# Kernel optimization log

Hardware: AMD Instinct MI355X
Metric: run time of the kernel (lower is better)

Reference implementation:

```python
import jax, jax.numpy as jnp
import numpy as np

B, S, D, H = 4, 2048, 1024, 16
DH = D // H
NEG = -1e9


def setup_inputs() -> dict:
    key = jax.random.key(0)
    ks = jax.random.split(key, 6)
    return {
        "q_raw": jax.random.normal(ks[0], (B, S, D), jnp.float32),
        "kv_raw": jax.random.normal(ks[1], (B, S, D), jnp.float32),
        "padding_mask": jnp.ones((B, S), jnp.int32),
        "Wq": jax.random.normal(ks[2], (D, D), jnp.float32) * 0.02,
        "Wk": jax.random.normal(ks[3], (D, D), jnp.float32) * 0.02,
        "Wv": jax.random.normal(ks[4], (D, D), jnp.float32) * 0.02,
        "Wo": jax.random.normal(ks[5], (D, D), jnp.float32) * 0.02,
    }


def _split_heads(x):
    # (B, S, D) -> (B, H, S, DH)
    return x.reshape(B, S, H, DH).transpose(0, 2, 1, 3)


def reference(q_raw, kv_raw, padding_mask, Wq, Wk, Wv, Wo):
    # nn.Linear (no bias): y = x @ W.T
    q = _split_heads(q_raw @ Wq.T)
    k = _split_heads(kv_raw @ Wk.T)
    v = _split_heads(kv_raw @ Wv.T)

    scale = 1.0 / jnp.sqrt(jnp.float32(DH))
    scores = jnp.einsum("bhqd,bhkd->bhqk", q, k) * scale  # (B,H,S,S)

    # padding mask: 0 -> masked (broadcast over query dim), as in torch code
    pad = (padding_mask == 0)[:, None, None, :]  # (B,1,1,S)
    scores = jnp.where(pad, NEG, scores)
    # causal mask (only applied when padding_mask given, matching original)
    causal = jnp.triu(jnp.ones((S, S), bool), k=1)  # (S,S)
    scores = jnp.where(causal[None, None], NEG, scores)

    w = jax.nn.softmax(scores, axis=-1)
    att = jnp.einsum("bhqk,bhkd->bhqd", w, v)  # (B,H,S,DH)
    att = att.transpose(0, 2, 1, 3).reshape(B, S, D)
    return att @ Wo.T
```

## Files before the change

kernel.cpp:

```cpp
#include <hip/hip_runtime.h>
#include <stdint.h>

typedef __attribute__((ext_vector_type(8))) short  short8;
typedef __attribute__((ext_vector_type(4))) float  f32x4;
typedef __attribute__((ext_vector_type(4))) unsigned short us4;

static __device__ __forceinline__ unsigned short f2bf(float x) {
  unsigned u = __builtin_bit_cast(unsigned, x);
  u += 0x7FFFu + ((u >> 16) & 1u);
  return (unsigned short)(u >> 16);
}

static __device__ __forceinline__ unsigned cvt_pk_bf16(float lo, float hi) {
  unsigned r;
  asm("v_cvt_pk_bf16_f32 %0, %1, %2" : "=v"(r) : "v"(lo), "v"(hi));
  return r;
}

template <int CTRL>
static __device__ __forceinline__ float maxdpp(float v) {
  int o = __builtin_amdgcn_update_dpp(0, __builtin_bit_cast(int, v), CTRL, 0xf, 0xf, false);
  return fmaxf(v, __builtin_bit_cast(float, o));
}
static __device__ __forceinline__ float rowmax16(float v) {
  v = maxdpp<0xB1>(v);
  v = maxdpp<0x4E>(v);
  v = maxdpp<0x141>(v);
  v = maxdpp<0x140>(v);
  return v;
}

__global__ __launch_bounds__(256) void cvt6(const float* __restrict__ q_raw,
                                            const float* __restrict__ kv_raw,
                                            const float* __restrict__ Wq,
                                            const float* __restrict__ Wk,
                                            const float* __restrict__ Wv,
                                            const float* __restrict__ Wo,
                                            unsigned short* __restrict__ qbf,
                                            unsigned short* __restrict__ kvbf,
                                            unsigned short* __restrict__ wbf) {
  const int y = blockIdx.y;
  const float* in;
  unsigned short* out;
  int n4;
  if (y == 0)      { in = q_raw;  out = qbf;  n4 = 2097152; }
  else if (y == 1) { in = kv_raw; out = kvbf; n4 = 2097152; }
  else {
    in  = (y == 2) ? Wq : (y == 3) ? Wk : (y == 4) ? Wv : Wo;
    out = wbf + (size_t)(y - 2) * 1048576;
    n4 = 262144;
  }
  int i = blockIdx.x * 256 + threadIdx.x;
  const int stride = gridDim.x * 256;
  for (; i < n4; i += stride) {
    f32x4 v = *((const f32x4*)in + i);
    us4 o = { f2bf(v[0]), f2bf(v[1]), f2bf(v[2]), f2bf(v[3]) };
    *((us4*)out + i) = o;
  }
}

__global__ __launch_bounds__(1024) void bias_kernel(const int* __restrict__ pm,
                                                    float* __restrict__ bias,
                                                    unsigned* __restrict__ flagmask) {
  __shared__ unsigned m;
  const int b = blockIdx.x, tid = threadIdx.x;
  if (tid == 0) m = 0;
  __syncthreads();
  const int i0 = b * 2048 + tid;
  const int z0 = pm[i0], z1 = pm[i0 + 1024];
  bias[i0]        = z0 ? 0.f : -1.0e9f;
  bias[i0 + 1024] = z1 ? 0.f : -1.0e9f;
  const int wv = tid >> 6;
  unsigned long long b0 = __ballot(z0 == 0);
  unsigned long long b1 = __ballot(z1 == 0);
  if ((tid & 63) == 0) {
    unsigned bits = (b0 ? (1u << wv) : 0u) | (b1 ? (1u << (wv + 16)) : 0u);
    if (bits) atomicOr(&m, bits);
  }
  __syncthreads();
  if (tid == 0) flagmask[b] = m;
}

static __device__ __forceinline__ void g2l16(const void* g, void* l) {
  __builtin_amdgcn_global_load_lds(
      (const __attribute__((address_space(1))) void*)g,
      (__attribute__((address_space(3))) void*)l, 16, 0, 0);
}

__global__ __launch_bounds__(256) void gemm_proj(const unsigned short* __restrict__ qbf,
                                                 const unsigned short* __restrict__ kvbf,
                                                 const unsigned short* __restrict__ wbf,
                                                 unsigned short* __restrict__ Qp,
                                                 unsigned short* __restrict__ Kp,
                                                 unsigned short* __restrict__ Vtp,
                                                 float qscale) {
  __shared__ unsigned short Alds[128 * 32];
  __shared__ unsigned short Blds[128 * 32];
  const int tid  = threadIdx.x;
  const int lane = tid & 63;
  const int w    = tid >> 6;
  const int g    = lane >> 4;
  const int li   = lane & 15;
  const int x = blockIdx.x;
  const int region = x >> 3;
  const int n0 = (x & 7) * 128;
  const int m0 = blockIdx.y * 128;
  const int wm = (w >> 1) * 64;
  const int wn = (w & 1) * 64;

  const unsigned short* A = (region == 0) ? qbf : kvbf;
  const unsigned short* W = wbf + (size_t)region * 1048576;

  int aoff[4], boff[4];
#pragma unroll
  for (int mi = 0; mi < 4; ++mi) {
    int row = wm + mi * 16 + li;
    aoff[mi] = row * 32 + (g ^ ((row >> 1) & 3)) * 8;
  }
#pragma unroll
  for (int ni = 0; ni < 4; ++ni) {
    int col = wn + ni * 16 + li;
    boff[ni] = col * 32 + (g ^ ((col >> 1) & 3)) * 8;
  }

  const int s1 = tid, s2 = 256 + tid;
  const int r1 = s1 >> 2, gc1 = (s1 & 3) ^ ((r1 >> 1) & 3);
  const int r2 = s2 >> 2, gc2 = (s2 & 3) ^ ((r2 >> 1) & 3);
  const unsigned short* gA1 = A + (size_t)(m0 + r1) * 1024 + gc1 * 8;
  const unsigned short* gA2 = A + (size_t)(m0 + r2) * 1024 + gc2 * 8;
  const unsigned short* gB1 = W + (size_t)(n0 + r1) * 1024 + gc1 * 8;
  const unsigned short* gB2 = W + (size_t)(n0 + r2) * 1024 + gc2 * 8;
  unsigned short* lA1 = &Alds[w * 512];
  unsigned short* lA2 = &Alds[2048 + w * 512];
  unsigned short* lB1 = &Blds[w * 512];
  unsigned short* lB2 = &Blds[2048 + w * 512];

  f32x4 acc[4][4] = {};

#pragma unroll 1
  for (int kt = 0; kt < 32; ++kt) {
    g2l16(gA1, lA1); g2l16(gA2, lA2);
    g2l16(gB1, lB1); g2l16(gB2, lB2);
    gA1 += 32; gA2 += 32; gB1 += 32; gB2 += 32;
    asm volatile("s_waitcnt vmcnt(0)" ::: "memory");
    __syncthreads();
    short8 af[4], bf[4];
#pragma unroll
    for (int mi = 0; mi < 4; ++mi) af[mi] = *(const short8*)&Alds[aoff[mi]];
#pragma unroll
    for (int ni = 0; ni < 4; ++ni) bf[ni] = *(const short8*)&Blds[boff[ni]];
#pragma unroll
    for (int mi = 0; mi < 4; ++mi)
#pragma unroll
      for (int ni = 0; ni < 4; ++ni)
        acc[mi][ni] = __builtin_amdgcn_mfma_f32_16x16x32_bf16(af[mi], bf[ni], acc[mi][ni], 0, 0, 0);
    __syncthreads();
  }

  if (region == 2) {
#pragma unroll
    for (int mi = 0; mi < 4; ++mi) {
      int mb = m0 + wm + mi * 16 + g * 4;
      int bb = mb >> 11, s = mb & 2047;
#pragma unroll
      for (int ni = 0; ni < 4; ++ni) {
        int n = n0 + wn + ni * 16 + li;
        us4 pk = { f2bf(acc[mi][ni][0]), f2bf(acc[mi][ni][1]),
                   f2bf(acc[mi][ni][2]), f2bf(acc[mi][ni][3]) };
        *(us4*)&Vtp[(size_t)(bb * 1024 + n) * 2048 + s] = pk;
      }
    }
  } else {
    unsigned short* C = (region == 0) ? Qp : Kp;
    const float sc = (region == 0) ? qscale : 1.0f;
#pragma unroll
    for (int mi = 0; mi < 4; ++mi) {
      int mb = m0 + wm + mi * 16 + g * 4;
#pragma unroll
      for (int ni = 0; ni < 4; ++ni) {
        int n = n0 + wn + ni * 16 + li;
#pragma unroll
        for (int r = 0; r < 4; ++r)
          C[(size_t)(mb + r) * 1024 + n] = f2bf(acc[mi][ni][r] * sc);
      }
    }
  }
}

__global__ __launch_bounds__(256) void gemm_out(const unsigned short* __restrict__ A,
                                                const unsigned short* __restrict__ W,
                                                float* __restrict__ C) {
  __shared__ unsigned short Alds[128 * 32];
  __shared__ unsigned short Blds[128 * 32];
  const int tid  = threadIdx.x;
  const int lane = tid & 63;
  const int w    = tid >> 6;
  const int g    = lane >> 4;
  const int li   = lane & 15;
  const int m0 = blockIdx.y * 128;
  const int n0 = blockIdx.x * 128;
  const int wm = (w >> 1) * 64;
  const int wn = (w & 1) * 64;

  int aoff[4], boff[4];
#pragma unroll
  for (int mi = 0; mi < 4; ++mi) {
    int row = wm + mi * 16 + li;
    aoff[mi] = row * 32 + (g ^ ((row >> 1) & 3)) * 8;
  }
#pragma unroll
  for (int ni = 0; ni < 4; ++ni) {
    int col = wn + ni * 16 + li;
    boff[ni] = col * 32 + (g ^ ((col >> 1) & 3)) * 8;
  }

  const int s1 = tid, s2 = 256 + tid;
  const int r1 = s1 >> 2, gc1 = (s1 & 3) ^ ((r1 >> 1) & 3);
  const int r2 = s2 >> 2, gc2 = (s2 & 3) ^ ((r2 >> 1) & 3);
  const unsigned short* gA1 = A + (size_t)(m0 + r1) * 1024 + gc1 * 8;
  const unsigned short* gA2 = A + (size_t)(m0 + r2) * 1024 + gc2 * 8;
  const unsigned short* gB1 = W + (size_t)(n0 + r1) * 1024 + gc1 * 8;
  const unsigned short* gB2 = W + (size_t)(n0 + r2) * 1024 + gc2 * 8;
  unsigned short* lA1 = &Alds[w * 512];
  unsigned short* lA2 = &Alds[2048 + w * 512];
  unsigned short* lB1 = &Blds[w * 512];
  unsigned short* lB2 = &Blds[2048 + w * 512];

  f32x4 acc[4][4] = {};

#pragma unroll 1
  for (int kt = 0; kt < 32; ++kt) {
    g2l16(gA1, lA1); g2l16(gA2, lA2);
    g2l16(gB1, lB1); g2l16(gB2, lB2);
    gA1 += 32; gA2 += 32; gB1 += 32; gB2 += 32;
    asm volatile("s_waitcnt vmcnt(0)" ::: "memory");
    __syncthreads();
    short8 af[4], bf[4];
#pragma unroll
    for (int mi = 0; mi < 4; ++mi) af[mi] = *(const short8*)&Alds[aoff[mi]];
#pragma unroll
    for (int ni = 0; ni < 4; ++ni) bf[ni] = *(const short8*)&Blds[boff[ni]];
#pragma unroll
    for (int mi = 0; mi < 4; ++mi)
#pragma unroll
      for (int ni = 0; ni < 4; ++ni)
        acc[mi][ni] = __builtin_amdgcn_mfma_f32_16x16x32_bf16(af[mi], bf[ni], acc[mi][ni], 0, 0, 0);
    __syncthreads();
  }

#pragma unroll
  for (int mi = 0; mi < 4; ++mi) {
    int mb = m0 + wm + mi * 16 + g * 4;
#pragma unroll
    for (int ni = 0; ni < 4; ++ni) {
      int n = n0 + wn + ni * 16 + li;
#pragma unroll
      for (int r = 0; r < 4; ++r)
        C[(size_t)(mb + r) * 1024 + n] = acc[mi][ni][r];
    }
  }
}

__global__ __launch_bounds__(256, 4) void attn_kernel(const unsigned short* __restrict__ Qp,
                                                      const unsigned short* __restrict__ Kp,
                                                      const unsigned short* __restrict__ Vt,
                                                      const float* __restrict__ bias,
                                                      const unsigned* __restrict__ flagmask,
                                                      unsigned short* __restrict__ att) {
  __shared__ unsigned short Klds[2][64 * 64];
  __shared__ unsigned short Vlds[2][64 * 64];
  __shared__ unsigned short Plds[4][16 * 64];

  const int tid = threadIdx.x, lane = tid & 63, w = tid >> 6;
  const int g = lane >> 4, li = lane & 15;

  const int rid = blockIdx.x + (blockIdx.y << 4);
  const int xcd = rid & 7, kk = rid >> 3;
  const int bh = (kk & 7) | (xcd << 3);
  const int b = bh >> 4, h = bh & 15;
  const int tA = kk >> 3, tB = 31 - tA;
  const int nA = tA + 1, nB = tB + 1;

  const unsigned smask = flagmask[b];

  const int s1 = tid, s2 = tid + 256;
  const int r1 = s1 >> 3, c1 = (s1 & 7) ^ (r1 & 7);
  const int r2 = s2 >> 3, c2 = (s2 & 7) ^ (r2 & 7);
  const unsigned short* Kb1 = Kp + (size_t)(b * 2048 + r1) * 1024 + h * 64 + c1 * 8;
  const unsigned short* Kb2 = Kp + (size_t)(b * 2048 + r2) * 1024 + h * 64 + c2 * 8;
  const unsigned short* Vb1 = Vt + (size_t)(b * 1024 + h * 64 + r1) * 2048 + c1 * 8;
  const unsigned short* Vb2 = Vt + (size_t)(b * 1024 + h * 64 + r2) * 2048 + c2 * 8;

  int foff[2][4];
#pragma unroll
  for (int ks = 0; ks < 2; ++ks)
#pragma unroll
    for (int i = 0; i < 4; ++i)
      foff[ks][i] = (i * 16 + li) * 64 + (((ks * 4 + g) ^ (li & 7)) * 8);

  unsigned short* Pl = &Plds[w][0];
  const int swr = (li & 7) ^ (li >> 3);
  int poff[2];
#pragma unroll
  for (int ks = 0; ks < 2; ++ks) poff[ks] = li * 64 + ((ks * 4 + g) ^ swr) * 8;

  const float* bbase = bias + b * 2048 + li;

  short8 ones;
#pragma unroll
  for (int j = 0; j < 8; ++j) ones[j] = (short)0x3F80;

  int qw = tA * 64 + w * 16;
  short8 qfr[2];
#pragma unroll
  for (int ks = 0; ks < 2; ++ks)
    qfr[ks] = *(const short8*)&Qp[((size_t)(b * 2048 + qw + li)) * 1024 +
                                  h * 64 + ks * 32 + g * 8];

  f32x4 acco[4] = {};
  f32x4 lacc = {};
  float mrow[4] = {-3.0e38f, -3.0e38f, -3.0e38f, -3.0e38f};
  const f32x4 Z = {0.f, 0.f, 0.f, 0.f};

  auto stage = [&](int kt, int bufn) {
    const size_t ko = (size_t)kt * 65536, vo = (size_t)kt * 64;
    g2l16(Kb1 + ko, &Klds[bufn][w * 512]);
    g2l16(Kb2 + ko, &Klds[bufn][2048 + w * 512]);
    g2l16(Vb1 + vo, &Vlds[bufn][w * 512]);
    g2l16(Vb2 + vo, &Vlds[bufn][2048 + w * 512]);
  };

  auto body = [&](int kt, bool diag, int buf) {
    f32x4 s[4];
#pragma unroll
    for (int ni = 0; ni < 4; ++ni) {
      short8 kf = *(const short8*)&Klds[buf][foff[0][ni]];
      s[ni] = __builtin_amdgcn_mfma_f32_16x16x32_bf16(qfr[0], kf, Z, 0, 0, 0);
    }
#pragma unroll
    for (int ni = 0; ni < 4; ++ni) {
      short8 kf = *(const short8*)&Klds[buf][foff[1][ni]];
      s[ni] = __builtin_amdgcn_mfma_f32_16x16x32_bf16(qfr[1], kf, s[ni], 0, 0, 0);
    }
    if ((smask >> kt) & 1u) {
#pragma unroll
      for (int ni = 0; ni < 4; ++ni) {
        float bv = bbase[kt * 64 + ni * 16];
#pragma unroll
        for (int r = 0; r < 4; ++r) s[ni][r] += bv;
      }
    }
    if (diag) {
      const int q0 = qw + g * 4;
#pragma unroll
      for (int ni = 0; ni < 4; ++ni) {
        const int key = kt * 64 + ni * 16 + li;
#pragma unroll
        for (int r = 0; r < 4; ++r)
          if (key > q0 + r) s[ni][r] = -1.0e9f;
      }
    }
    float tm[4];
#pragma unroll
    for (int r = 0; r < 4; ++r)
      tm[r] = rowmax16(fmaxf(fmaxf(s[0][r], s[1][r]), fmaxf(s[2][r], s[3][r])));
    int need = 0;
#pragma unroll
    for (int r = 0; r < 4; ++r) need |= (tm[r] > mrow[r] + 8.0f) ? 1 : 0;
    if (__any(need)) {
#pragma unroll
      for (int r = 0; r < 4; ++r) {
        const float mn = fmaxf(mrow[r], tm[r]);
        const float al = __builtin_amdgcn_exp2f(mrow[r] - mn);
        mrow[r] = mn;
        lacc[r] *= al;
#pragma unroll
        for (int df = 0; df < 4; ++df) acco[df][r] *= al;
      }
    }
#pragma unroll
    for (int ni = 0; ni < 4; ++ni) {
#pragma unroll
      for (int h2 = 0; h2 < 2; ++h2) {
        float lo = __builtin_amdgcn_exp2f(s[ni][2 * h2]     - mrow[2 * h2]);
        float hi = __builtin_amdgcn_exp2f(s[ni][2 * h2 + 1] - mrow[2 * h2 + 1]);
        unsigned pk = cvt_pk_bf16(lo, hi);
        const int r0 = g * 4 + 2 * h2;
        const int ch = 2 * ni + (li >> 3);
        const int lo7 = li & 7;
        Pl[r0 * 64 + ((ch ^ ((r0 & 7) ^ (g >> 1))) * 8) + lo7] = (unsigned short)pk;
        const int rr = r0 + 1;
        Pl[rr * 64 + ((ch ^ ((rr & 7) ^ (g >> 1))) * 8) + lo7] = (unsigned short)(pk >> 16);
      }
    }
#pragma unroll
    for (int ks = 0; ks < 2; ++ks) {
      const short8 pa = *(const short8*)&Pl[poff[ks]];
      short8 vf[4];
#pragma unroll
      for (int df = 0; df < 4; ++df) vf[df] = *(const short8*)&Vlds[buf][foff[ks][df]];
#pragma unroll
      for (int df = 0; df < 4; ++df)
        acco[df] = __builtin_amdgcn_mfma_f32_16x16x32_bf16(pa, vf[df], acco[df], 0, 0, 0);
      lacc = __builtin_amdgcn_mfma_f32_16x16x32_bf16(pa, ones, lacc, 0, 0, 0);
    }
  };

  auto epilogue = [&]() {
    float inv[4];
#pragma unroll
    for (int r = 0; r < 4; ++r) inv[r] = __builtin_amdgcn_rcpf(lacc[r]);
    const int qb0 = qw + g * 4;
#pragma unroll
    for (int df = 0; df < 4; ++df) {
      const int d = h * 64 + df * 16 + li;
#pragma unroll
      for (int r = 0; r < 4; ++r)
        att[(size_t)(b * 2048 + qb0 + r) * 1024 + d] = f2bf(acco[df][r] * inv[r]);
    }
  };

  stage(0, 0);
  int buf = 0;

#pragma unroll 1
  for (int kt = 0; kt < nA; ++kt) {
    stage((kt + 1 < nA) ? kt + 1 : 0, buf ^ 1);
    asm volatile("s_waitcnt vmcnt(4)" ::: "memory");
    __builtin_amdgcn_s_barrier();
    body(kt, kt == nA - 1, buf);
    __builtin_amdgcn_s_barrier();
    buf ^= 1;
  }

  epilogue();
  qw = tB * 64 + w * 16;
#pragma unroll
  for (int ks = 0; ks < 2; ++ks)
    qfr[ks] = *(const short8*)&Qp[((size_t)(b * 2048 + qw + li)) * 1024 +
                                  h * 64 + ks * 32 + g * 8];
#pragma unroll
  for (int df = 0; df < 4; ++df) acco[df] = Z;
  lacc = Z;
#pragma unroll
  for (int r = 0; r < 4; ++r) mrow[r] = -3.0e38f;

#pragma unroll 1
  for (int kt = 0; kt < nB; ++kt) {
    if (kt + 1 < nB) {
      stage(kt + 1, buf ^ 1);
      asm volatile("s_waitcnt vmcnt(4)" ::: "memory");
    } else {
      asm volatile("s_waitcnt vmcnt(0)" ::: "memory");
    }
    __builtin_amdgcn_s_barrier();
    body(kt, kt == nB - 1, buf);
    __builtin_amdgcn_s_barrier();
    buf ^= 1;
  }

  epilogue();
}

extern "C" void kernel_launch(void* const* d_in, const int* in_sizes, int n_in,
                              void* d_out, int out_size, void* d_ws, size_t ws_size,
                              hipStream_t stream) {
  const float* q_raw  = (const float*)d_in[0];
  const float* kv_raw = (const float*)d_in[1];
  const int*   pmask  = (const int*)d_in[2];
  const float* Wq = (const float*)d_in[3];
  const float* Wk = (const float*)d_in[4];
  const float* Wv = (const float*)d_in[5];
  const float* Wo = (const float*)d_in[6];
  float* out = (float*)d_out;

  const size_t NEL = 8388608;
  const size_t WEL = 1048576;
  unsigned short* ws   = (unsigned short*)d_ws;
  unsigned short* qbf  = ws;
  unsigned short* kvbf = qbf + NEL;
  unsigned short* wbf  = kvbf + NEL;
  unsigned short* Qp   = wbf + 4 * WEL;
  unsigned short* Kp   = Qp + NEL;
  unsigned short* Vtp  = Kp + NEL;
  float*          bias = (float*)(Vtp + NEL);
  unsigned*       flagmask = (unsigned*)(bias + 8192);
  unsigned short* att  = qbf;

  const float sc = 0.125f * 1.44269504088896340736f;

  cvt6<<<dim3(512, 6), 256, 0, stream>>>(q_raw, kv_raw, Wq, Wk, Wv, Wo, qbf, kvbf, wbf);
  bias_kernel<<<4, 1024, 0, stream>>>(pmask, bias, flagmask);
  gemm_proj<<<dim3(24, 64), 256, 0, stream>>>(qbf, kvbf, wbf, Qp, Kp, Vtp, sc);
  attn_kernel<<<dim3(16, 64), 256, 0, stream>>>(Qp, Kp, Vtp, bias, flagmask, att);
  gemm_out<<<dim3(8, 64), 256, 0, stream>>>(att, wbf + 3 * WEL, out);
}
```

Baseline: 211.4 us.

## Double-buffer GEMM LDS loads and remap blocks for XCD-local L2 reuse

```diff
diff --git a/kernel.cpp b/kernel.cpp
--- a/kernel.cpp
+++ b/kernel.cpp
@@ -94,17 +94,20 @@
                                                  unsigned short* __restrict__ Kp,
                                                  unsigned short* __restrict__ Vtp,
                                                  float qscale) {
-  __shared__ unsigned short Alds[128 * 32];
-  __shared__ unsigned short Blds[128 * 32];
+  __shared__ unsigned short Alds[2][4096];
+  __shared__ unsigned short Blds[2][4096];
   const int tid  = threadIdx.x;
   const int lane = tid & 63;
   const int w    = tid >> 6;
   const int g    = lane >> 4;
   const int li   = lane & 15;
-  const int x = blockIdx.x;
-  const int region = x >> 3;
-  const int n0 = (x & 7) * 128;
-  const int m0 = blockIdx.y * 128;
+
+  const int l = blockIdx.x;
+  const int xcd = l & 7, j = l >> 3;
+  const int mstep = j & 7, rn = j >> 3;
+  const int region = rn >> 3;
+  const int n0 = (rn & 7) * 128;
+  const int m0 = (xcd * 8 + mstep) * 128;
   const int wm = (w >> 1) * 64;
   const int wn = (w & 1) * 64;
 
@@ -130,31 +133,37 @@
   const unsigned short* gA2 = A + (size_t)(m0 + r2) * 1024 + gc2 * 8;
   const unsigned short* gB1 = W + (size_t)(n0 + r1) * 1024 + gc1 * 8;
   const unsigned short* gB2 = W + (size_t)(n0 + r2) * 1024 + gc2 * 8;
-  unsigned short* lA1 = &Alds[w * 512];
-  unsigned short* lA2 = &Alds[2048 + w * 512];
-  unsigned short* lB1 = &Blds[w * 512];
-  unsigned short* lB2 = &Blds[2048 + w * 512];
 
   f32x4 acc[4][4] = {};
 
+  g2l16(gA1, &Alds[0][w * 512]); g2l16(gA2, &Alds[0][2048 + w * 512]);
+  g2l16(gB1, &Blds[0][w * 512]); g2l16(gB2, &Blds[0][2048 + w * 512]);
+  gA1 += 32; gA2 += 32; gB1 += 32; gB2 += 32;
+
+  int cur = 0;
 #pragma unroll 1
   for (int kt = 0; kt < 32; ++kt) {
-    g2l16(gA1, lA1); g2l16(gA2, lA2);
-    g2l16(gB1, lB1); g2l16(gB2, lB2);
-    gA1 += 32; gA2 += 32; gB1 += 32; gB2 += 32;
-    asm volatile("s_waitcnt vmcnt(0)" ::: "memory");
-    __syncthreads();
+    if (kt < 31) {
+      g2l16(gA1, &Alds[cur ^ 1][w * 512]); g2l16(gA2, &Alds[cur ^ 1][2048 + w * 512]);
+      g2l16(gB1, &Blds[cur ^ 1][w * 512]); g2l16(gB2, &Blds[cur ^ 1][2048 + w * 512]);
+      gA1 += 32; gA2 += 32; gB1 += 32; gB2 += 32;
+      asm volatile("s_waitcnt vmcnt(4)" ::: "memory");
+    } else {
+      asm volatile("s_waitcnt vmcnt(0)" ::: "memory");
+    }
+    __builtin_amdgcn_s_barrier();
     short8 af[4], bf[4];
 #pragma unroll
-    for (int mi = 0; mi < 4; ++mi) af[mi] = *(const short8*)&Alds[aoff[mi]];
-#pragma unroll
-    for (int ni = 0; ni < 4; ++ni) bf[ni] = *(const short8*)&Blds[boff[ni]];
+    for (int mi = 0; mi < 4; ++mi) af[mi] = *(const short8*)&Alds[cur][aoff[mi]];
+#pragma unroll
+    for (int ni = 0; ni < 4; ++ni) bf[ni] = *(const short8*)&Blds[cur][boff[ni]];
 #pragma unroll
     for (int mi = 0; mi < 4; ++mi)
 #pragma unroll
       for (int ni = 0; ni < 4; ++ni)
         acc[mi][ni] = __builtin_amdgcn_mfma_f32_16x16x32_bf16(af[mi], bf[ni], acc[mi][ni], 0, 0, 0);
-    __syncthreads();
+    __builtin_amdgcn_s_barrier();
+    cur ^= 1;
   }
 
   if (region == 2) {
@@ -190,15 +199,19 @@
 __global__ __launch_bounds__(256) void gemm_out(const unsigned short* __restrict__ A,
                                                 const unsigned short* __restrict__ W,
                                                 float* __restrict__ C) {
-  __shared__ unsigned short Alds[128 * 32];
-  __shared__ unsigned short Blds[128 * 32];
+  __shared__ unsigned short Alds[2][4096];
+  __shared__ unsigned short Blds[2][4096];
   const int tid  = threadIdx.x;
   const int lane = tid & 63;
   const int w    = tid >> 6;
   const int g    = lane >> 4;
   const int li   = lane & 15;
-  const int m0 = blockIdx.y * 128;
-  const int n0 = blockIdx.x * 128;
+
+  const int l = blockIdx.x;
+  const int xcd = l & 7, j = l >> 3;
+  const int mstep = j & 7, nt = j >> 3;
+  const int m0 = (xcd * 8 + mstep) * 128;
+  const int n0 = nt * 128;
   const int wm = (w >> 1) * 64;
   const int wn = (w & 1) * 64;
 
@@ -221,31 +234,37 @@
   const unsigned short* gA2 = A + (size_t)(m0 + r2) * 1024 + gc2 * 8;
   const unsigned short* gB1 = W + (size_t)(n0 + r1) * 1024 + gc1 * 8;
   const unsigned short* gB2 = W + (size_t)(n0 + r2) * 1024 + gc2 * 8;
-  unsigned short* lA1 = &Alds[w * 512];
-  unsigned short* lA2 = &Alds[2048 + w * 512];
-  unsigned short* lB1 = &Blds[w * 512];
-  unsigned short* lB2 = &Blds[2048 + w * 512];
 
   f32x4 acc[4][4] = {};
 
+  g2l16(gA1, &Alds[0][w * 512]); g2l16(gA2, &Alds[0][2048 + w * 512]);
+  g2l16(gB1, &Blds[0][w * 512]); g2l16(gB2, &Blds[0][2048 + w * 512]);
+  gA1 += 32; gA2 += 32; gB1 += 32; gB2 += 32;
+
+  int cur = 0;
 #pragma unroll 1
   for (int kt = 0; kt < 32; ++kt) {
-    g2l16(gA1, lA1); g2l16(gA2, lA2);
-    g2l16(gB1, lB1); g2l16(gB2, lB2);
-    gA1 += 32; gA2 += 32; gB1 += 32; gB2 += 32;
-    asm volatile("s_waitcnt vmcnt(0)" ::: "memory");
-    __syncthreads();
+    if (kt < 31) {
+      g2l16(gA1, &Alds[cur ^ 1][w * 512]); g2l16(gA2, &Alds[cur ^ 1][2048 + w * 512]);
+      g2l16(gB1, &Blds[cur ^ 1][w * 512]); g2l16(gB2, &Blds[cur ^ 1][2048 + w * 512]);
+      gA1 += 32; gA2 += 32; gB1 += 32; gB2 += 32;
+      asm volatile("s_waitcnt vmcnt(4)" ::: "memory");
+    } else {
+      asm volatile("s_waitcnt vmcnt(0)" ::: "memory");
+    }
+    __builtin_amdgcn_s_barrier();
     short8 af[4], bf[4];
 #pragma unroll
-    for (int mi = 0; mi < 4; ++mi) af[mi] = *(const short8*)&Alds[aoff[mi]];
-#pragma unroll
-    for (int ni = 0; ni < 4; ++ni) bf[ni] = *(const short8*)&Blds[boff[ni]];
+    for (int mi = 0; mi < 4; ++mi) af[mi] = *(const short8*)&Alds[cur][aoff[mi]];
+#pragma unroll
+    for (int ni = 0; ni < 4; ++ni) bf[ni] = *(const short8*)&Blds[cur][boff[ni]];
 #pragma unroll
     for (int mi = 0; mi < 4; ++mi)
 #pragma unroll
       for (int ni = 0; ni < 4; ++ni)
         acc[mi][ni] = __builtin_amdgcn_mfma_f32_16x16x32_bf16(af[mi], bf[ni], acc[mi][ni], 0, 0, 0);
-    __syncthreads();
+    __builtin_amdgcn_s_barrier();
+    cur ^= 1;
   }
 
 #pragma unroll
@@ -308,7 +327,7 @@
 
   short8 ones;
 #pragma unroll
-  for (int j = 0; j < 8; ++j) ones[j] = (short)0x3F80;
+  for (int j2 = 0; j2 < 8; ++j2) ones[j2] = (short)0x3F80;
 
   int qw = tA * 64 + w * 16;
   short8 qfr[2];
@@ -491,7 +510,7 @@
 
   cvt6<<<dim3(512, 6), 256, 0, stream>>>(q_raw, kv_raw, Wq, Wk, Wv, Wo, qbf, kvbf, wbf);
   bias_kernel<<<4, 1024, 0, stream>>>(pmask, bias, flagmask);
-  gemm_proj<<<dim3(24, 64), 256, 0, stream>>>(qbf, kvbf, wbf, Qp, Kp, Vtp, sc);
+  gemm_proj<<<1536, 256, 0, stream>>>(qbf, kvbf, wbf, Qp, Kp, Vtp, sc);
   attn_kernel<<<dim3(16, 64), 256, 0, stream>>>(Qp, Kp, Vtp, bias, flagmask, att);
-  gemm_out<<<dim3(8, 64), 256, 0, stream>>>(att, wbf + 3 * WEL, out);
-}
+  gemm_out<<<512, 256, 0, stream>>>(att, wbf + 3 * WEL, out);
+}
```

New measurement: 191.2 us. -9.6%, faster.
